# Performance work log

Measured on AMD Instinct MI355X. Metric: run time of the kernel, lower is better.

The kernel has to match this reference:

```python
import jax, jax.numpy as jnp
import numpy as np

ENC_DIM = 1024
EMB_DIM = 256
K = 8192          # codebook size
COMMIT = 0.25
LN_EPS = 1e-5


def _ln(x, g, b):
    m = jnp.mean(x, axis=-1, keepdims=True)
    v = jnp.mean(jnp.square(x - m), axis=-1, keepdims=True)
    return (x - m) * jax.lax.rsqrt(v + LN_EPS) * g + b


def _mlp(x, W1, b1, g1, be1, W2, b2, g2, be2):
    # two feed_forward blocks: Linear -> ReLU -> LayerNorm
    x = _ln(jax.nn.relu(x @ W1 + b1), g1, be1)
    x = _ln(jax.nn.relu(x @ W2 + b2), g2, be2)
    return x


def setup_inputs() -> dict:
    key = jax.random.key(0)
    ks = jax.random.split(key, 10)
    d = ENC_DIM
    s = 1.0 / np.sqrt(d)
    inp = {"x": jax.random.normal(ks[0], (4, 2048, d), dtype=jnp.float32)}
    # encoder MLP (2 blocks)
    inp["We1"] = jax.random.uniform(ks[1], (d, d), jnp.float32, -s, s)
    inp["be1"] = jnp.zeros((d,), jnp.float32)
    inp["ge1"] = jnp.ones((d,), jnp.float32)
    inp["bne1"] = jnp.zeros((d,), jnp.float32)
    inp["We2"] = jax.random.uniform(ks[2], (d, d), jnp.float32, -s, s)
    inp["be2"] = jnp.zeros((d,), jnp.float32)
    inp["ge2"] = jnp.ones((d,), jnp.float32)
    inp["bne2"] = jnp.zeros((d,), jnp.float32)
    # decoder MLP (2 blocks)
    inp["Wd1"] = jax.random.uniform(ks[3], (d, d), jnp.float32, -s, s)
    inp["bd1"] = jnp.zeros((d,), jnp.float32)
    inp["gd1"] = jnp.ones((d,), jnp.float32)
    inp["bnd1"] = jnp.zeros((d,), jnp.float32)
    inp["Wd2"] = jax.random.uniform(ks[4], (d, d), jnp.float32, -s, s)
    inp["bd2"] = jnp.zeros((d,), jnp.float32)
    inp["gd2"] = jnp.ones((d,), jnp.float32)
    inp["bnd2"] = jnp.zeros((d,), jnp.float32)
    # codebook, init uniform(-1/K, 1/K)
    inp["codebook"] = jax.random.uniform(ks[5], (K, EMB_DIM), jnp.float32, -1.0 / K, 1.0 / K)
    return inp


def reference(x, We1, be1, ge1, bne1, We2, be2, ge2, bne2,
              Wd1, bd1, gd1, bnd1, Wd2, bd2, gd2, bnd2, codebook):
    bs, seq_len, d = x.shape
    z = _mlp(x, We1, be1, ge1, bne1, We2, be2, ge2, bne2)

    # ---- VectorQuantizer ----
    zg = z.reshape(bs, seq_len, -1, EMB_DIM)              # (b, s, g, e)
    flat = zg.reshape(-1, EMB_DIM)                        # (N, e)
    # pairwise squared distances to codebook: (N, K)
    dist = (jnp.sum(flat * flat, axis=1, keepdims=True)
            + jnp.sum(codebook * codebook, axis=1)
            - 2.0 * flat @ codebook.T)
    idx = jnp.argmin(dist, axis=1)                        # (N,)
    quantized = jnp.take(codebook, idx, axis=0).reshape(zg.shape)

    e_latent = jnp.mean(jnp.square(jax.lax.stop_gradient(quantized) - zg))
    q_latent = jnp.mean(jnp.square(quantized - jax.lax.stop_gradient(zg)))
    loss = q_latent + COMMIT * e_latent

    # straight-through estimator
    quantized = zg + jax.lax.stop_gradient(quantized - zg)
    quantized = quantized.reshape(bs, seq_len, d)

    # perplexity from code usage histogram
    n = flat.shape[0]
    counts = jnp.zeros((K,), x.dtype).at[idx].add(1.0)
    avg_probs = counts / n
    perplexity = jnp.exp(-jnp.sum(avg_probs * jnp.log(avg_probs + 1e-10)))

    out = _mlp(quantized, Wd1, bd1, gd1, bnd1, Wd2, bd2, gd2, bnd2)
    return (out, loss, perplexity)
```

## Files before the change

### kernel.cpp

```cpp
#include <hip/hip_runtime.h>
#include <stdint.h>


typedef short bf16x8 __attribute__((ext_vector_type(8)));
typedef float f32x4 __attribute__((ext_vector_type(4)));

__device__ __forceinline__ void gl2lds16(const void* g, void* l) {
  __builtin_amdgcn_global_load_lds(
      (const __attribute__((address_space(1))) void*)g,
      (__attribute__((address_space(3))) void*)l, 16, 0, 0);
}

__device__ __forceinline__ float bf2f(unsigned short u) {
  return __uint_as_float(((unsigned)u) << 16);
}
__device__ __forceinline__ unsigned short f2bf(float f) {
  unsigned x = __float_as_uint(f);
  unsigned r = (x + 0x7fffu + ((x >> 16) & 1u)) >> 16;
  return (unsigned short)r;
}
__device__ __forceinline__ unsigned long long packScore(float s, int code) {
  unsigned u = __float_as_uint(s);
  u = (u & 0x80000000u) ? ~u : (u | 0x80000000u);
  return ((unsigned long long)u << 32) | (unsigned)code;
}
__device__ __forceinline__ unsigned long long shflxor_u64(unsigned long long v, int m) {
  union { unsigned long long u; int i[2]; } a;
  a.u = v;
  a.i[0] = __shfl_xor(a.i[0], m);
  a.i[1] = __shfl_xor(a.i[1], m);
  return a.u;
}

__global__ __launch_bounds__(256)
void cast_bf16(const float* __restrict__ X, unsigned short* __restrict__ Y, int n4) {
  int i = blockIdx.x * 256 + threadIdx.x;
  if (i < n4) {
    float4 v = ((const float4*)X)[i];
    ushort4 o = make_ushort4(f2bf(v.x), f2bf(v.y), f2bf(v.z), f2bf(v.w));
    ((ushort4*)Y)[i] = o;
  }
}

__global__ __launch_bounds__(256)
void transpose_cast(const float* __restrict__ W, unsigned short* __restrict__ Wt, int D) {
  __shared__ float s[32][33];
  int tx = threadIdx.x & 31, ty = threadIdx.x >> 5;
  int bx = blockIdx.x, by = blockIdx.y;
#pragma unroll
  for (int p = 0; p < 4; p++) {
    int r = by * 32 + ty + p * 8, c = bx * 32 + tx;
    s[ty + p * 8][tx] = W[(size_t)r * D + c];
  }
  __syncthreads();
#pragma unroll
  for (int p = 0; p < 4; p++) {
    int r = bx * 32 + ty + p * 8, c = by * 32 + tx;
    Wt[(size_t)r * D + c] = f2bf(s[tx][ty + p * 8]);
  }
}

__global__ __launch_bounds__(256)
void code_norms(const float* __restrict__ cb, float* __restrict__ cn) {
  int row = blockIdx.x * 4 + (threadIdx.x >> 6);
  int lane = threadIdx.x & 63;
  float4 v = ((const float4*)(cb + (size_t)row * 256))[lane];
  float s = v.x * v.x + v.y * v.y + v.z * v.z + v.w * v.w;
#pragma unroll
  for (int off = 32; off > 0; off >>= 1) s += __shfl_down(s, off);
  if (lane == 0) cn[row] = s;
}

__global__ __launch_bounds__(256, 2)
void gemm_bias_relu(const unsigned short* __restrict__ A, const unsigned short* __restrict__ Bt,
                    const float* __restrict__ bias, unsigned short* __restrict__ C,
                    int M, int N, int K) {
  __shared__ unsigned short As[128 * 64];
  __shared__ unsigned short Bs[128 * 64];
  const int t = threadIdx.x;
  const int wv = t >> 6, lane = t & 63;
  const int wm = wv >> 1, wn = wv & 1;
  const int quad = lane >> 4, l15 = lane & 15;
  const int row0 = blockIdx.y * 128, col0 = blockIdx.x * 128;
  const int rsub = lane >> 3;
  const int dchunk = (lane & 7) ^ rsub;

  f32x4 acc[4][4];
#pragma unroll
  for (int i = 0; i < 4; i++)
#pragma unroll
    for (int j = 0; j < 4; j++) acc[i][j] = (f32x4){0.f, 0.f, 0.f, 0.f};

  for (int k0 = 0; k0 < K; k0 += 64) {
#pragma unroll
    for (int j = 0; j < 4; j++) {
      int slab = j * 4 + wv;
      int row = slab * 8 + rsub;
      gl2lds16(A + (size_t)(row0 + row) * K + k0 + dchunk * 8, As + slab * 512);
      gl2lds16(Bt + (size_t)(col0 + row) * K + k0 + dchunk * 8, Bs + slab * 512);
    }
    __syncthreads();
#pragma unroll
    for (int kk = 0; kk < 2; kk++) {
      bf16x8 af[4], bfr[4];
#pragma unroll
      for (int mt = 0; mt < 4; mt++) {
        int row = wm * 64 + mt * 16 + l15;
        af[mt] = *(const bf16x8*)(As + row * 64 + (((kk * 4 + quad) ^ (l15 & 7)) * 8));
      }
#pragma unroll
      for (int nt = 0; nt < 4; nt++) {
        int row = wn * 64 + nt * 16 + l15;
        bfr[nt] = *(const bf16x8*)(Bs + row * 64 + (((kk * 4 + quad) ^ (l15 & 7)) * 8));
      }
#pragma unroll
      for (int mt = 0; mt < 4; mt++)
#pragma unroll
        for (int nt = 0; nt < 4; nt++)
          acc[mt][nt] = __builtin_amdgcn_mfma_f32_16x16x32_bf16(af[mt], bfr[nt], acc[mt][nt], 0, 0, 0);
    }
    __syncthreads();
  }
#pragma unroll
  for (int mt = 0; mt < 4; mt++) {
#pragma unroll
    for (int nt = 0; nt < 4; nt++) {
      int col = col0 + wn * 64 + nt * 16 + l15;
      float b = bias[col];
#pragma unroll
      for (int r = 0; r < 4; r++) {
        int row = row0 + wm * 64 + mt * 16 + quad * 4 + r;
        float v = acc[mt][nt][r] + b;
        C[(size_t)row * N + col] = f2bf(v > 0.f ? v : 0.f);
      }
    }
  }
}

__global__ __launch_bounds__(256)
void ln_kernel(const unsigned short* __restrict__ X, const float* __restrict__ g,
               const float* __restrict__ b, unsigned short* __restrict__ obf,
               float* __restrict__ of32) {
  const int row = blockIdx.x, t = threadIdx.x;
  ushort4 u = ((const ushort4*)(X + (size_t)row * 1024))[t];
  float4 v = make_float4(bf2f(u.x), bf2f(u.y), bf2f(u.z), bf2f(u.w));
  float s = v.x + v.y + v.z + v.w;
  float ss = v.x * v.x + v.y * v.y + v.z * v.z + v.w * v.w;
#pragma unroll
  for (int off = 32; off > 0; off >>= 1) {
    s += __shfl_down(s, off);
    ss += __shfl_down(ss, off);
  }
  __shared__ float rs[4], rss[4];
  const int wave = t >> 6, lane = t & 63;
  if (lane == 0) { rs[wave] = s; rss[wave] = ss; }
  __syncthreads();
  float S = rs[0] + rs[1] + rs[2] + rs[3];
  float SS = rss[0] + rss[1] + rss[2] + rss[3];
  float m = S * (1.0f / 1024.0f);
  float var = SS * (1.0f / 1024.0f) - m * m;
  float rstd = 1.0f / sqrtf(var + 1e-5f);
  float4 gv = ((const float4*)g)[t];
  float4 bv = ((const float4*)b)[t];
  float4 o;
  o.x = (v.x - m) * rstd * gv.x + bv.x;
  o.y = (v.y - m) * rstd * gv.y + bv.y;
  o.z = (v.z - m) * rstd * gv.z + bv.z;
  o.w = (v.w - m) * rstd * gv.w + bv.w;
  if (obf) {
    ushort4 q = make_ushort4(f2bf(o.x), f2bf(o.y), f2bf(o.z), f2bf(o.w));
    ((ushort4*)(obf + (size_t)row * 1024))[t] = q;
  } else {
    ((float4*)(of32 + (size_t)row * 1024))[t] = o;
  }
}

__global__ __launch_bounds__(256, 2)
void vq_dist(const unsigned short* __restrict__ Z, const unsigned short* __restrict__ Cb,
             const float* __restrict__ cnorm, unsigned long long* __restrict__ bestg) {
  __shared__ unsigned short Bs[2][64 * 256];
  __shared__ unsigned long long runmin[64];
  const int t = threadIdx.x;
  const int wv = t >> 6, lane = t & 63;
  const int quad = lane >> 4, l15 = lane & 15;
  const int row0 = blockIdx.x * 64;

  if (t < 64) runmin[t] = ~0ull;

  bf16x8 zf[4][8];
#pragma unroll
  for (int mt = 0; mt < 4; mt++)
#pragma unroll
    for (int ks = 0; ks < 8; ks++)
      zf[mt][ks] = *(const bf16x8*)(Z + (size_t)(row0 + mt * 16 + l15) * 256 + ks * 32 + quad * 8);

  float msc[4][4];
  int mcd[4][4];
#pragma unroll
  for (int mt = 0; mt < 4; mt++)
#pragma unroll
    for (int r = 0; r < 4; r++) { msc[mt][r] = 3.4e38f; mcd[mt][r] = 0; }

  const int dcode = lane >> 5;
  const int dgr = lane & 31;
  const int slot = wv * 16 + l15;
  const int rxor = l15 & 7;

  unsigned swz[8];
#pragma unroll
  for (int ks = 0; ks < 8; ks++)
    swz[ks] = (unsigned)slot * 256 + (unsigned)(((ks * 4 + quad) ^ rxor) * 8);

#pragma unroll
  for (int j = 0; j < 8; j++) {
    int slab = wv * 8 + j;
    int sl = slab * 2 + dcode;
    gl2lds16(Cb + (size_t)sl * 256 + ((dgr ^ (sl & 7)) * 8), &Bs[0][slab * 512]);
  }
  float cn_old = 3.4e38f;
  float cn_new = cnorm[slot];

  f32x4 pacc[4];
#pragma unroll
  for (int mt = 0; mt < 4; mt++) pacc[mt] = (f32x4){0.f, 0.f, 0.f, 0.f};

  for (int ch = 0; ch < 128; ch++) {
    const int cur = ch & 1;
    __builtin_amdgcn_s_waitcnt(0x3F70);

    {
      const int cb2 = ((ch + 1) & 127) * 64;
#pragma unroll
      for (int j = 0; j < 8; j++) {
        int slab = wv * 8 + j;
        int sl = slab * 2 + dcode;
        gl2lds16(Cb + (size_t)(cb2 + sl) * 256 + ((dgr ^ (sl & 7)) * 8),
                 &Bs[cur ^ 1][slab * 512]);
      }
    }

    const unsigned short* bsc = &Bs[cur][0];
    bf16x8 lbuf[8];
#pragma unroll
    for (int ks = 0; ks < 8; ks++)
      lbuf[ks] = *(const bf16x8*)(bsc + swz[ks]);

    {
      int code = (ch - 1) * 64 + slot;
#pragma unroll
      for (int mt = 0; mt < 4; mt++)
#pragma unroll
        for (int r = 0; r < 4; r++) {
          float sc = cn_old - 2.0f * pacc[mt][r];
          if (sc < msc[mt][r]) { msc[mt][r] = sc; mcd[mt][r] = code; }
        }
    }
    cn_old = cn_new;
    cn_new = cnorm[(((ch + 1) & 127) * 64) + slot];

    __builtin_amdgcn_s_setprio(1);
#pragma unroll
    for (int ks = 0; ks < 8; ks++) {
      if (ks == 0) {
        const f32x4 z4 = (f32x4){0.f, 0.f, 0.f, 0.f};
#pragma unroll
        for (int mt = 0; mt < 4; mt++)
          pacc[mt] = __builtin_amdgcn_mfma_f32_16x16x32_bf16(zf[mt][0], lbuf[0], z4, 0, 0, 0);
      } else {
#pragma unroll
        for (int mt = 0; mt < 4; mt++)
          pacc[mt] = __builtin_amdgcn_mfma_f32_16x16x32_bf16(zf[mt][ks], lbuf[ks], pacc[mt], 0, 0, 0);
      }
    }
    __builtin_amdgcn_s_setprio(0);
  }
  {
    int code = 127 * 64 + slot;
#pragma unroll
    for (int mt = 0; mt < 4; mt++)
#pragma unroll
      for (int r = 0; r < 4; r++) {
        float sc = cn_old - 2.0f * pacc[mt][r];
        if (sc < msc[mt][r]) { msc[mt][r] = sc; mcd[mt][r] = code; }
      }
  }

  __syncthreads();
#pragma unroll
  for (int mt = 0; mt < 4; mt++) {
#pragma unroll
    for (int r = 0; r < 4; r++) {
      unsigned long long bp = packScore(msc[mt][r], mcd[mt][r]);
#pragma unroll
      for (int m = 1; m < 16; m <<= 1) {
        unsigned long long o = shflxor_u64(bp, m);
        bp = o < bp ? o : bp;
      }
      if (l15 == 0) atomicMin(&runmin[mt * 16 + quad * 4 + r], bp);
    }
  }
  __syncthreads();
  if (t < 64) bestg[row0 + t] = runmin[t];
}

__global__ __launch_bounds__(256)
void vq_gather(const unsigned long long* __restrict__ bestg, const float* __restrict__ cb,
               const unsigned short* __restrict__ zb, unsigned short* __restrict__ qb,
               int* __restrict__ counts, float* __restrict__ lpart) {
  const int wave = threadIdx.x >> 6;
  const int g = blockIdx.x * 4 + wave;
  const int lane = threadIdx.x & 63;
  const int idx = (int)(bestg[g] & 0xFFFFFFFFull);
  float4 c = ((const float4*)(cb + (size_t)idx * 256))[lane];
  ushort4 q = make_ushort4(f2bf(c.x), f2bf(c.y), f2bf(c.z), f2bf(c.w));
  ((ushort4*)(qb + (size_t)g * 256))[lane] = q;
  ushort4 z = ((const ushort4*)(zb + (size_t)g * 256))[lane];
  float dx = c.x - bf2f(z.x), dy = c.y - bf2f(z.y);
  float dz = c.z - bf2f(z.z), dw = c.w - bf2f(z.w);
  float p = dx * dx + dy * dy + dz * dz + dw * dw;
#pragma unroll
  for (int off = 32; off > 0; off >>= 1) p += __shfl_down(p, off);
  __shared__ float sp[4];
  if (lane == 0) {
    sp[wave] = p;
    atomicAdd(&counts[idx], 1);
  }
  __syncthreads();
  if (threadIdx.x == 0) lpart[blockIdx.x] = sp[0] + sp[1] + sp[2] + sp[3];
}

__global__ __launch_bounds__(256)
void finalize(const int* __restrict__ counts, const float* __restrict__ lpart,
              float* __restrict__ out2) {
  const int t = threadIdx.x;
  double h = 0.0, l = 0.0;
  for (int i = t; i < 8192; i += 256) {
    double pr = (double)counts[i] * (1.0 / 32768.0);
    h += pr * log(pr + 1e-10);
    l += (double)lpart[i];
  }
  __shared__ double sh[256], sl[256];
  sh[t] = h;
  sl[t] = l;
  __syncthreads();
  for (int w = 128; w > 0; w >>= 1) {
    if (t < w) { sh[t] += sh[t + w]; sl[t] += sl[t + w]; }
    __syncthreads();
  }
  if (t == 0) {
    out2[0] = (float)(1.25 * sl[0] * (1.0 / 8388608.0));
    out2[1] = (float)exp(-sh[0]);
  }
}

extern "C" void kernel_launch(void* const* d_in, const int* in_sizes, int n_in,
                              void* d_out, int out_size, void* d_ws, size_t ws_size,
                              hipStream_t stream) {
  const float* x = (const float*)d_in[0];
  const float* We1 = (const float*)d_in[1];
  const float* be1 = (const float*)d_in[2];
  const float* ge1 = (const float*)d_in[3];
  const float* bne1 = (const float*)d_in[4];
  const float* We2 = (const float*)d_in[5];
  const float* be2 = (const float*)d_in[6];
  const float* ge2 = (const float*)d_in[7];
  const float* bne2 = (const float*)d_in[8];
  const float* Wd1 = (const float*)d_in[9];
  const float* bd1 = (const float*)d_in[10];
  const float* gd1 = (const float*)d_in[11];
  const float* bnd1 = (const float*)d_in[12];
  const float* Wd2 = (const float*)d_in[13];
  const float* bd2 = (const float*)d_in[14];
  const float* gd2 = (const float*)d_in[15];
  const float* bnd2 = (const float*)d_in[16];
  const float* codebook = (const float*)d_in[17];
  float* out = (float*)d_out;

  char* w = (char*)d_ws;
  auto alloc = [&](size_t bytes) -> char* {
    char* p = w;
    w += (bytes + 255) & ~(size_t)255;
    return p;
  };
  unsigned short* xb = (unsigned short*)alloc((size_t)8192 * 1024 * 2);
  unsigned short* wt0 = (unsigned short*)alloc((size_t)1024 * 1024 * 2);
  unsigned short* wt1 = (unsigned short*)alloc((size_t)1024 * 1024 * 2);
  unsigned short* wt2 = (unsigned short*)alloc((size_t)1024 * 1024 * 2);
  unsigned short* wt3 = (unsigned short*)alloc((size_t)1024 * 1024 * 2);
  unsigned short* cbb = (unsigned short*)alloc((size_t)8192 * 256 * 2);
  float* cnorm = (float*)alloc((size_t)8192 * 4);
  unsigned short* act = (unsigned short*)alloc((size_t)8192 * 1024 * 2);
  unsigned short* yb = (unsigned short*)alloc((size_t)8192 * 1024 * 2);
  unsigned short* zb = (unsigned short*)alloc((size_t)8192 * 1024 * 2);
  unsigned short* qb = (unsigned short*)alloc((size_t)8192 * 1024 * 2);
  unsigned long long* best = (unsigned long long*)alloc((size_t)32768 * 8);
  int* counts = (int*)alloc((size_t)8192 * 4);
  float* lpart = (float*)alloc((size_t)8192 * 4);

  hipMemsetAsync(counts, 0, (size_t)8192 * 4, stream);

  cast_bf16<<<(2097152 + 255) / 256, 256, 0, stream>>>(x, xb, 2097152);
  dim3 tg(32, 32);
  transpose_cast<<<tg, 256, 0, stream>>>(We1, wt0, 1024);
  transpose_cast<<<tg, 256, 0, stream>>>(We2, wt1, 1024);
  transpose_cast<<<tg, 256, 0, stream>>>(Wd1, wt2, 1024);
  transpose_cast<<<tg, 256, 0, stream>>>(Wd2, wt3, 1024);
  cast_bf16<<<(524288 + 255) / 256, 256, 0, stream>>>(codebook, cbb, 524288);
  code_norms<<<2048, 256, 0, stream>>>(codebook, cnorm);

  dim3 gg(8, 64);
  gemm_bias_relu<<<gg, 256, 0, stream>>>(xb, wt0, be1, act, 8192, 1024, 1024);
  ln_kernel<<<8192, 256, 0, stream>>>(act, ge1, bne1, yb, nullptr);
  gemm_bias_relu<<<gg, 256, 0, stream>>>(yb, wt1, be2, act, 8192, 1024, 1024);
  ln_kernel<<<8192, 256, 0, stream>>>(act, ge2, bne2, zb, nullptr);
  vq_dist<<<512, 256, 0, stream>>>(zb, cbb, cnorm, best);
  vq_gather<<<8192, 256, 0, stream>>>(best, codebook, zb, qb, counts, lpart);
  gemm_bias_relu<<<gg, 256, 0, stream>>>(qb, wt2, bd1, act, 8192, 1024, 1024);
  ln_kernel<<<8192, 256, 0, stream>>>(act, gd1, bnd1, yb, nullptr);
  gemm_bias_relu<<<gg, 256, 0, stream>>>(yb, wt3, bd2, act, 8192, 1024, 1024);
  ln_kernel<<<8192, 256, 0, stream>>>(act, gd2, bnd2, nullptr, out);

  finalize<<<1, 256, 0, stream>>>(counts, lpart, out + 8388608);
}
```

Before: 447.7 us.

## Load codebook fragments directly from global into registers, drop LDS staging

The VQ distance kernel stops staging codebook tiles in a double-buffered shared-memory array through async global-to-LDS loads. Each lane now reads its own bf16 codebook fragments straight from global memory into registers, prefetching the next chunk in two halves interleaved with the MFMA sequence. This removes the LDS round trip, the waitcnt stalls and the LDS footprint, which may allow more resident blocks. In exchange each wave issues its own global loads of the same codebook rows and depends on L2/L1 hits and on register double buffering to hide latency.

```diff
diff --git a/kernel.cpp b/kernel.cpp
--- a/kernel.cpp
+++ b/kernel.cpp
@@ -178,7 +178,6 @@
 __global__ __launch_bounds__(256, 2)
 void vq_dist(const unsigned short* __restrict__ Z, const unsigned short* __restrict__ Cb,
              const float* __restrict__ cnorm, unsigned long long* __restrict__ bestg) {
-  __shared__ unsigned short Bs[2][64 * 256];
   __shared__ unsigned long long runmin[64];
   const int t = threadIdx.x;
   const int wv = t >> 6, lane = t & 63;
@@ -201,22 +200,13 @@
 #pragma unroll
     for (int r = 0; r < 4; r++) { msc[mt][r] = 3.4e38f; mcd[mt][r] = 0; }
 
-  const int dcode = lane >> 5;
-  const int dgr = lane & 31;
   const int slot = wv * 16 + l15;
-  const int rxor = l15 & 7;
-
-  unsigned swz[8];
+  const unsigned short* gbase = Cb + (size_t)slot * 256 + quad * 8;
+
+  bf16x8 lbuf[8];
 #pragma unroll
   for (int ks = 0; ks < 8; ks++)
-    swz[ks] = (unsigned)slot * 256 + (unsigned)(((ks * 4 + quad) ^ rxor) * 8);
-
-#pragma unroll
-  for (int j = 0; j < 8; j++) {
-    int slab = wv * 8 + j;
-    int sl = slab * 2 + dcode;
-    gl2lds16(Cb + (size_t)sl * 256 + ((dgr ^ (sl & 7)) * 8), &Bs[0][slab * 512]);
-  }
+    lbuf[ks] = *(const bf16x8*)(gbase + ks * 32);
   float cn_old = 3.4e38f;
   float cn_new = cnorm[slot];
 
@@ -225,26 +215,6 @@
   for (int mt = 0; mt < 4; mt++) pacc[mt] = (f32x4){0.f, 0.f, 0.f, 0.f};
 
   for (int ch = 0; ch < 128; ch++) {
-    const int cur = ch & 1;
-    __builtin_amdgcn_s_waitcnt(0x3F70);
-
-    {
-      const int cb2 = ((ch + 1) & 127) * 64;
-#pragma unroll
-      for (int j = 0; j < 8; j++) {
-        int slab = wv * 8 + j;
-        int sl = slab * 2 + dcode;
-        gl2lds16(Cb + (size_t)(cb2 + sl) * 256 + ((dgr ^ (sl & 7)) * 8),
-                 &Bs[cur ^ 1][slab * 512]);
-      }
-    }
-
-    const unsigned short* bsc = &Bs[cur][0];
-    bf16x8 lbuf[8];
-#pragma unroll
-    for (int ks = 0; ks < 8; ks++)
-      lbuf[ks] = *(const bf16x8*)(bsc + swz[ks]);
-
     {
       int code = (ch - 1) * 64 + slot;
 #pragma unroll
@@ -258,21 +228,32 @@
     cn_old = cn_new;
     cn_new = cnorm[(((ch + 1) & 127) * 64) + slot];
 
+    const size_t nb = (size_t)((ch + 1) & 127) * 16384;
+
     __builtin_amdgcn_s_setprio(1);
-#pragma unroll
-    for (int ks = 0; ks < 8; ks++) {
-      if (ks == 0) {
-        const f32x4 z4 = (f32x4){0.f, 0.f, 0.f, 0.f};
-#pragma unroll
-        for (int mt = 0; mt < 4; mt++)
-          pacc[mt] = __builtin_amdgcn_mfma_f32_16x16x32_bf16(zf[mt][0], lbuf[0], z4, 0, 0, 0);
-      } else {
+    {
+      const f32x4 z4 = (f32x4){0.f, 0.f, 0.f, 0.f};
+#pragma unroll
+      for (int mt = 0; mt < 4; mt++)
+        pacc[mt] = __builtin_amdgcn_mfma_f32_16x16x32_bf16(zf[mt][0], lbuf[0], z4, 0, 0, 0);
+#pragma unroll
+      for (int ks = 1; ks < 4; ks++)
 #pragma unroll
         for (int mt = 0; mt < 4; mt++)
           pacc[mt] = __builtin_amdgcn_mfma_f32_16x16x32_bf16(zf[mt][ks], lbuf[ks], pacc[mt], 0, 0, 0);
-      }
-    }
+    }
+#pragma unroll
+    for (int ks = 0; ks < 4; ks++)
+      lbuf[ks] = *(const bf16x8*)(gbase + nb + ks * 32);
+#pragma unroll
+    for (int ks = 4; ks < 8; ks++)
+#pragma unroll
+      for (int mt = 0; mt < 4; mt++)
+        pacc[mt] = __builtin_amdgcn_mfma_f32_16x16x32_bf16(zf[mt][ks], lbuf[ks], pacc[mt], 0, 0, 0);
     __builtin_amdgcn_s_setprio(0);
+#pragma unroll
+    for (int ks = 4; ks < 8; ks++)
+      lbuf[ks] = *(const bf16x8*)(gbase + nb + ks * 32);
   }
   {
     int code = 127 * 64 + slot;
```

New measurement: 545.0 us. +21.7%, slower.
